# Kernel optimization log

Measured on AMD Instinct MI355X. Metric: run time of the kernel, lower is better.

## Reference

```python
import jax, jax.numpy as jnp
import numpy as np

B, T, N, F, H = 64, 50, 24, 256, 256  # batch, timesteps, graph nodes, input feat, hidden


def setup_inputs() -> dict:
    key = jax.random.key(0)
    ks = jax.random.split(key, 12)
    sF = 1.0 / np.sqrt(F)
    sH = 1.0 / np.sqrt(H)
    u = lambda k, shape, s: jax.random.uniform(k, shape, jnp.float32, -s, s)
    return {
        "x": jax.random.normal(ks[0], (B, T, N, F), jnp.float32),
        "G": jax.random.normal(ks[1], (N, N), jnp.float32) / np.sqrt(N),
        "W_ih": u(ks[2], (4 * H, F), sF),
        "b_ih": u(ks[3], (4 * H,), sF),
        "W_hh": u(ks[4], (4 * H, H), sH),
        "b_hh": u(ks[5], (4 * H,), sH),
        "W_h1": u(ks[6], (H, F), sF),
        "b_h1": u(ks[7], (H,), sF),
        "W_h2": u(ks[8], (H, F), sF),
        "b_h2": u(ks[9], (H,), sF),
        "W_fc": u(ks[10], (H, H), sH),
        "b_fc": u(ks[11], (H,), sH),
    }


def graph_linear(G, x, W, b):
    # GraphLinear: node-mixing G then feature projection W, bias after mixing
    # x: [B, N, f_in] -> [B, N, f_out]
    return jnp.einsum('nm,bmf->bnf', G, x @ W.T) + b


def reference(x, G, W_ih, b_ih, W_hh, b_hh, W_h1, b_h1, W_h2, b_h2, W_fc, b_fc):
    x0 = x[:, 0]                                   # [B, N, F]
    h = graph_linear(G, x0, W_h1, b_h1)            # initial hidden
    c = graph_linear(G, x0, W_h2, b_h2)            # initial cell

    def step(carry, xt):
        h, c = carry
        gates = (graph_linear(G, xt, W_ih, b_ih)
                 + graph_linear(G, h, W_hh, b_hh))  # [B, N, 4H]
        i, f, g, o = jnp.split(gates, 4, axis=-1)
        c = jax.nn.sigmoid(f) * c + jax.nn.sigmoid(i) * jnp.tanh(g)
        h = jax.nn.sigmoid(o) * jnp.tanh(c)
        return (h, c), None

    (h, c), _ = jax.lax.scan(step, (h, c), jnp.swapaxes(x, 0, 1))  # scan over T
    # dropout(p=0.0) is identity; final projection + tanh on last timestep output
    return jnp.tanh(graph_linear(G, h, W_fc, b_fc))
```

## Files before the change

kernel.cpp:

```cpp
#include <hip/hip_runtime.h>
#include <stdint.h>

#define T_ 50

typedef float f32x4 __attribute__((ext_vector_type(4)));
typedef short s16x8 __attribute__((ext_vector_type(8)));
typedef uint64_t u64x2 __attribute__((ext_vector_type(2)));

#define WS_WIH   0u
#define WS_WHH   524288u
#define WS_WINIT 1048576u
#define WS_WFC   1310720u
#define WS_GPAD  1441792u
#define WS_FLG   1443840u
#define WS_NEED  1460224u

#define L_WHH  0
#define L_A2   131072
#define L_XL   143360
#define L_ZR   155840
#define L_HST  156352
#define L_HST2 160448
#define L_TOT  163520

__device__ __forceinline__ f32x4 mfma16(s16x8 a, s16x8 b, f32x4 c){
  return __builtin_amdgcn_mfma_f32_16x16x32_bf16(a, b, c, 0, 0, 0);
}
__device__ __forceinline__ uint32_t bfbits(float f){
  uint32_t u = __builtin_bit_cast(uint32_t, f);
  u += 0x7FFFu + ((u >> 16) & 1u);
  return u >> 16;
}
__device__ __forceinline__ uint32_t pk2bf(float lo, float hi){
  return bfbits(lo) | (bfbits(hi) << 16);
}
#define LOG2E 1.4426950408889634f
__device__ __forceinline__ float fexp2(float x){ return __builtin_amdgcn_exp2f(x); }
__device__ __forceinline__ float frcp_(float x){ return __builtin_amdgcn_rcpf(x); }
__device__ __forceinline__ float fsig(float x){ return frcp_(1.f + fexp2(-LOG2E * x)); }
__device__ __forceinline__ float ftanh_(float x){ return 1.f - 2.f * frcp_(1.f + fexp2(2.f * LOG2E * x)); }

__global__ void prep_kernel(const float* __restrict__ G,
                            const float* __restrict__ Wih, const float* __restrict__ Whh,
                            const float* __restrict__ Wh1, const float* __restrict__ Wh2,
                            const float* __restrict__ Wfc, uint8_t* __restrict__ ws)
{
  const int tid = blockIdx.x * blockDim.x + threadIdx.x;
  const int nth = gridDim.x * blockDim.x;
  uint16_t* wih = (uint16_t*)(ws + WS_WIH);
  uint16_t* whh = (uint16_t*)(ws + WS_WHH);
  uint16_t* wini= (uint16_t*)(ws + WS_WINIT);
  uint16_t* wfc = (uint16_t*)(ws + WS_WFC);
  uint16_t* gp  = (uint16_t*)(ws + WS_GPAD);
  uint32_t* flg = (uint32_t*)(ws + WS_FLG);

  for (int i = tid; i < 262144; i += nth){
    int cg = i >> 16, c = (i >> 8) & 255, k = i & 255;
    int row = (c >> 6)*256 + 64*cg + (c & 63);
    wih[i] = (uint16_t)bfbits(Wih[row*256 + k]);
    whh[i] = (uint16_t)bfbits(Whh[row*256 + k]);
  }
  for (int i = tid; i < 131072; i += nth){
    int cg = i >> 15, c = (i >> 8) & 127, k = i & 255;
    float v = (c < 64) ? Wh1[(64*cg + c)*256 + k] : Wh2[(64*cg + c - 64)*256 + k];
    wini[i] = (uint16_t)bfbits(v);
  }
  for (int i = tid; i < 65536; i += nth){
    int cg = i >> 14, c = (i >> 8) & 63, k = i & 255;
    wfc[i] = (uint16_t)bfbits(Wfc[(64*cg + c)*256 + k]);
  }
  for (int i = tid; i < 1024; i += nth){
    int n = i >> 5, m = i & 31;
    gp[i] = (n < 24 && m < 24) ? (uint16_t)bfbits(G[n*24 + m]) : (uint16_t)0;
  }
  for (int i = tid; i < 4096; i += nth) flg[i] = 0;
}

__global__ void __launch_bounds__(512, 1)
encoder_kernel(const float* __restrict__ x, uint8_t* __restrict__ ws,
               float* __restrict__ out,
               const float* __restrict__ bih, const float* __restrict__ bhh,
               const float* __restrict__ bh1, const float* __restrict__ bh2,
               const float* __restrict__ bfc)
{
  extern __shared__ uint8_t smem[];
  uint16_t* WHHL = (uint16_t*)(smem + L_WHH);
  uint16_t* A2   = (uint16_t*)(smem + L_A2);
  uint16_t* XL   = (uint16_t*)(smem + L_XL);
  uint16_t* ZR   = (uint16_t*)(smem + L_ZR);
  uint16_t* HST  = (uint16_t*)(smem + L_HST);
  uint16_t* HST2 = (uint16_t*)(smem + L_HST2);

  const int tid = threadIdx.x;
  const int b   = blockIdx.x & 63;
  const int cg  = blockIdx.x >> 6;
  const int w   = tid >> 6;
  const int l   = tid & 63;
  const int l15 = l & 15;
  const int g   = l >> 4;
  const int Mt  = w >> 2;
  const int ns  = w & 3;
  const int ul  = ns*16 + l15;
  const int ug  = 64*cg + ul;

  const uint16_t* WIH  = (const uint16_t*)(ws + WS_WIH)   + (size_t)cg*65536;
  const uint16_t* WINI = (const uint16_t*)(ws + WS_WINIT) + (size_t)cg*32768;
  const uint16_t* WFC  = (const uint16_t*)(ws + WS_WFC)   + (size_t)cg*16384;
  const uint16_t* GP   = (const uint16_t*)(ws + WS_GPAD);
  uint32_t* flgB = (uint32_t*)(ws + WS_FLG) + b*64;
  uint32_t* flgW = flgB + cg*16;
  uint16_t* GhB  = (uint16_t*)((uint8_t*)out + (size_t)b*24576);

  {
    const uint8_t* src = ws + WS_WHH + (size_t)cg*131072;
    for (int i = tid*8; i < 65536; i += 4096){
      uint4 v = *(const uint4*)(src + (size_t)i*2);
      int col = i >> 8, k0 = i & 255;
      *(uint4*)&WHHL[col*256 + (k0 ^ ((col&7)<<3))] = v;
    }
  }
  for (int i = tid; i < 256;  i += 512) ZR[i] = 0;
  for (int i = tid; i < 2048; i += 512) HST[i] = 0;

  s16x8 gfragM = *(const s16x8*)&GP[(Mt*16 + l15)*32 + g*8];

  const float bb0 = bih[ug]     + bhh[ug];
  const float bb1 = bih[256+ug] + bhh[256+ug];
  const float bb2 = bih[512+ug] + bhh[512+ug];
  const float bb3 = bih[768+ug] + bhh[768+ug];
  const float bh1l = bh1[ug], bh2l = bh2[ug], bfcl = bfc[ug];

  const int arow = Mt*16 + l15;
  const int crow = (arow < 24) ? arow : 23;
  const uint16_t* a2row = (arow < 24) ? (A2 + arow*256) : ZR;
  const int sw = (arow < 24) ? ((arow & 7) << 3) : 0;

  auto xld_issue = [&](const float* xt, f32x4 xv[3]){
    #pragma unroll
    for (int p = 0; p < 3; p++)
      xv[p] = *(const f32x4*)(xt + tid*4 + p*2048);
  };
  auto xld_write = [&](const f32x4 xv[3]){
    #pragma unroll
    for (int p = 0; p < 3; p++){
      int e = tid*4 + p*2048;
      int m = e >> 8, f = e & 255;
      uint2 pk; pk.x = pk2bf(xv[p][0], xv[p][1]); pk.y = pk2bf(xv[p][2], xv[p][3]);
      *(uint2*)&XL[m*260 + f] = pk;
    }
  };

  auto gx_stage = [&](){
    #pragma unroll
    for (int jt = 0; jt < 4; jt++){
      int f = (jt*4 + ns)*16 + l15;
      s16x8 bfrag = (s16x8){0,0,0,0,0,0,0,0};
      if (g < 3){
        #pragma unroll
        for (int j = 0; j < 8; j++)
          bfrag[j] = (short)XL[(g*8 + j)*260 + f];
      }
      f32x4 zz = {0.f,0.f,0.f,0.f};
      f32x4 gx = mfma16(gfragM, bfrag, zz);
      int n0 = Mt*16 + g*4;
      if (n0 < 24){
        uint32_t a01 = pk2bf(gx[0], gx[1]), a23 = pk2bf(gx[2], gx[3]);
        A2[(n0  )*256 + (f ^ (((n0  )&7)<<3))] = (uint16_t)a01;
        A2[(n0+1)*256 + (f ^ (((n0+1)&7)<<3))] = (uint16_t)(a01>>16);
        A2[(n0+2)*256 + (f ^ (((n0+2)&7)<<3))] = (uint16_t)a23;
        A2[(n0+3)*256 + (f ^ (((n0+3)&7)<<3))] = (uint16_t)(a23>>16);
      }
    }
  };

  auto ghload = [&](int parity, unsigned long long af[8][2]){
    const unsigned long long* gs = (const unsigned long long*)(GhB + parity*6144);
    #pragma unroll
    for (int ks = 0; ks < 8; ks++){
      int e = crow*64 + ks*8 + g*2;
      af[ks][0] = __hip_atomic_load(gs + e,     __ATOMIC_RELAXED, __HIP_MEMORY_SCOPE_AGENT);
      af[ks][1] = __hip_atomic_load(gs + e + 1, __ATOMIC_RELAXED, __HIP_MEMORY_SCOPE_AGENT);
    }
  };

  auto wait_for = [&](uint32_t target){
    if (tid < 4){
      uint32_t* fp = flgB + tid*16;
      int guard = 0;
      while (__hip_atomic_load(fp, __ATOMIC_RELAXED, __HIP_MEMORY_SCOPE_AGENT) < target){
        __builtin_amdgcn_s_sleep(1);
        if (++guard > 20000000) break;
      }
    }
    __syncthreads();
  };

  auto do_publish = [&](const float hv[4], int parity, uint32_t flagval){
    int n0 = Mt*16 + g*4;
    if (n0 < 24){
      uint2 p; p.x = pk2bf(hv[0], hv[1]); p.y = pk2bf(hv[2], hv[3]);
      *(uint2*)&HST[ul*32 + n0] = p;
    }
    __syncthreads();
    s16x8 hb = *(const s16x8*)&HST[ul*32 + g*8];
    f32x4 zz = {0.f,0.f,0.f,0.f};
    f32x4 gh = mfma16(gfragM, hb, zz);
    if (n0 < 24){
      uint32_t q01 = pk2bf(gh[0], gh[1]), q23 = pk2bf(gh[2], gh[3]);
      HST2[(n0  )*64 + ul] = (uint16_t)q01;
      HST2[(n0+1)*64 + ul] = (uint16_t)(q01>>16);
      HST2[(n0+2)*64 + ul] = (uint16_t)q23;
      HST2[(n0+3)*64 + ul] = (uint16_t)(q23>>16);
    }
    __syncthreads();
    if (tid < 384){
      int node = tid >> 4, c4 = tid & 15;
      unsigned long long v = *(const unsigned long long*)&HST2[node*64 + c4*4];
      __hip_atomic_store((unsigned long long*)(GhB + parity*6144) + node*64 + cg*16 + c4,
                         v, __ATOMIC_RELAXED, __HIP_MEMORY_SCOPE_AGENT);
    }
    asm volatile("s_waitcnt vmcnt(0)" ::: "memory");
    __syncthreads();
    if (tid == 0)
      __hip_atomic_store(flgW, flagval, __ATOMIC_RELAXED, __HIP_MEMORY_SCOPE_AGENT);
  };

  float cst[4];
  f32x4 zacc[4];
  const float* xb = x + (size_t)b*T_*6144;

  {
    f32x4 xv[3];
    xld_issue(xb, xv);
    xld_write(xv);
  }
  __syncthreads();
  gx_stage();
  __syncthreads();
  {
    f32x4 h0a = {0.f,0.f,0.f,0.f}, c0a = {0.f,0.f,0.f,0.f};
    #pragma unroll
    for (int j = 0; j < 4; j++) zacc[j] = (f32x4){0.f,0.f,0.f,0.f};
    #pragma unroll
    for (int ks = 0; ks < 8; ks++){
      const int kk = ks*32 + g*8;
      s16x8 a  = *(const s16x8*)&a2row[kk ^ sw];
      s16x8 b1 = *(const s16x8*)&WINI[ul*256 + kk];
      s16x8 b2 = *(const s16x8*)&WINI[(64+ul)*256 + kk];
      h0a = mfma16(a, b1, h0a);
      c0a = mfma16(a, b2, c0a);
      #pragma unroll
      for (int j = 0; j < 4; j++){
        s16x8 bz = *(const s16x8*)&WIH[((j*4+ns)*16 + l15)*256 + kk];
        zacc[j] = mfma16(a, bz, zacc[j]);
      }
    }
    float hv0[4];
    #pragma unroll
    for (int r = 0; r < 4; r++){
      cst[r] = c0a[r] + bh2l;
      hv0[r] = h0a[r] + bh1l;
    }
    do_publish(hv0, 1, 1u);
  }
  {
    f32x4 xv[3];
    xld_issue(xb + 6144, xv);
    xld_write(xv);
    __syncthreads();
    gx_stage();
  }

  for (int t = 0; t < T_; t++){
    wait_for((uint32_t)(t+1));
    unsigned long long af[8][2];
    ghload((t+1)&1, af);

    f32x4 uacc[4];
    #pragma unroll
    for (int j = 0; j < 4; j++) uacc[j] = zacc[j];
    #pragma unroll
    for (int ks = 0; ks < 8; ks++){
      const int kk = ks*32 + g*8;
      u64x2 q; q.x = af[ks][0]; q.y = af[ks][1];
      s16x8 a = __builtin_bit_cast(s16x8, q);
      #pragma unroll
      for (int j = 0; j < 4; j++){
        int col = (j*4+ns)*16 + l15;
        s16x8 bf = *(const s16x8*)&WHHL[col*256 + (kk ^ ((col&7)<<3))];
        uacc[j] = mfma16(a, bf, uacc[j]);
      }
    }
    float hv[4];
    #pragma unroll
    for (int r = 0; r < 4; r++){
      float ig = fsig  (uacc[0][r] + bb0);
      float fg = fsig  (uacc[1][r] + bb1);
      float gg = ftanh_(uacc[2][r] + bb2);
      float og = fsig  (uacc[3][r] + bb3);
      float c  = fg*cst[r] + ig*gg;
      cst[r] = c;
      hv[r] = og*ftanh_(c);
    }
    do_publish(hv, t & 1, (uint32_t)(t+2));

    if (t+1 < T_){
      int tn = (t+2 < T_) ? (t+2) : (T_-1);
      f32x4 xv[3];
      xld_issue(xb + (size_t)tn*6144, xv);
      #pragma unroll
      for (int j = 0; j < 4; j++) zacc[j] = (f32x4){0.f,0.f,0.f,0.f};
      #pragma unroll
      for (int ks = 0; ks < 8; ks++){
        const int kk = ks*32 + g*8;
        s16x8 a = *(const s16x8*)&a2row[kk ^ sw];
        #pragma unroll
        for (int j = 0; j < 4; j++){
          s16x8 bf = *(const s16x8*)&WIH[((j*4+ns)*16 + l15)*256 + kk];
          zacc[j] = mfma16(a, bf, zacc[j]);
        }
      }
      __syncthreads();
      xld_write(xv);
      __syncthreads();
      gx_stage();
    }
  }

  wait_for((uint32_t)(T_+1));
  unsigned long long af[8][2];
  ghload(1, af);
  asm volatile("s_waitcnt vmcnt(0)" ::: "memory");
  __syncthreads();
  if (tid == 0)
    __hip_atomic_store(flgW, (uint32_t)(T_+2), __ATOMIC_RELAXED, __HIP_MEMORY_SCOPE_AGENT);
  wait_for((uint32_t)(T_+2));
  {
    f32x4 oacc = {0.f,0.f,0.f,0.f};
    #pragma unroll
    for (int ks = 0; ks < 8; ks++){
      const int kk = ks*32 + g*8;
      u64x2 q; q.x = af[ks][0]; q.y = af[ks][1];
      s16x8 a  = __builtin_bit_cast(s16x8, q);
      s16x8 bf = *(const s16x8*)&WFC[ul*256 + kk];
      oacc = mfma16(a, bf, oacc);
    }
    int n0 = Mt*16 + g*4;
    if (n0 < 24){
      #pragma unroll
      for (int r = 0; r < 4; r++)
        out[(size_t)b*6144 + (n0+r)*256 + ug] = ftanh_(oacc[r] + bfcl);
    }
  }
}

extern "C" void kernel_launch(void* const* d_in, const int* in_sizes, int n_in,
                              void* d_out, int out_size, void* d_ws, size_t ws_size,
                              hipStream_t stream)
{
  (void)in_sizes; (void)n_in; (void)out_size;
  if (ws_size < WS_NEED) return;

  const float* x   = (const float*)d_in[0];
  const float* G   = (const float*)d_in[1];
  const float* Wih = (const float*)d_in[2];
  const float* bih = (const float*)d_in[3];
  const float* Whh = (const float*)d_in[4];
  const float* bhh = (const float*)d_in[5];
  const float* Wh1 = (const float*)d_in[6];
  const float* bh1 = (const float*)d_in[7];
  const float* Wh2 = (const float*)d_in[8];
  const float* bh2 = (const float*)d_in[9];
  const float* Wfc = (const float*)d_in[10];
  const float* bfc = (const float*)d_in[11];
  uint8_t* ws = (uint8_t*)d_ws;
  float* outp = (float*)d_out;

  hipLaunchKernelGGL(prep_kernel, dim3(256), dim3(256), 0, stream,
                     G, Wih, Whh, Wh1, Wh2, Wfc, ws);

  hipFuncSetAttribute((const void*)encoder_kernel,
                      hipFuncAttributeMaxDynamicSharedMemorySize, L_TOT);
  void* args[] = {(void*)&x, (void*)&ws, (void*)&outp,
                  (void*)&bih, (void*)&bhh, (void*)&bh1, (void*)&bh2, (void*)&bfc};
  hipLaunchCooperativeKernel((const void*)encoder_kernel, dim3(256), dim3(512),
                             args, L_TOT, stream);
}
```

Measured before the change: 677.8 us.

## Replace flag-based inter-block sync with tagged per-element hidden-state exchange

Drops the separate flag array and the wait/publish barriers. Each published G·h value is now stored as a 32-bit word holding the bf16 value plus a step tag, so consumers poll the data itself until every tag matches. This removes the two __syncthreads, the vmcnt wait and the flag round-trip from each recurrent step, and it speculatively issues the next loads early. In exchange it doubles the exchange traffic, uses a larger workspace buffer zeroed in prep, and adds wave-wide tag checks and 32 loads per lane on every poll.

```diff
diff --git a/kernel.cpp b/kernel.cpp
--- a/kernel.cpp
+++ b/kernel.cpp
@@ -5,23 +5,21 @@
 
 typedef float f32x4 __attribute__((ext_vector_type(4)));
 typedef short s16x8 __attribute__((ext_vector_type(8)));
-typedef uint64_t u64x2 __attribute__((ext_vector_type(2)));
 
 #define WS_WIH   0u
 #define WS_WHH   524288u
 #define WS_WINIT 1048576u
 #define WS_WFC   1310720u
 #define WS_GPAD  1441792u
-#define WS_FLG   1443840u
-#define WS_NEED  1460224u
+#define WS_GHT   1443840u
+#define WS_NEED  4589568u
 
 #define L_WHH  0
 #define L_A2   131072
 #define L_XL   143360
 #define L_ZR   155840
 #define L_HST  156352
-#define L_HST2 160448
-#define L_TOT  163520
+#define L_TOT  160448
 
 __device__ __forceinline__ f32x4 mfma16(s16x8 a, s16x8 b, f32x4 c){
   return __builtin_amdgcn_mfma_f32_16x16x32_bf16(a, b, c, 0, 0, 0);
@@ -52,7 +50,7 @@
   uint16_t* wini= (uint16_t*)(ws + WS_WINIT);
   uint16_t* wfc = (uint16_t*)(ws + WS_WFC);
   uint16_t* gp  = (uint16_t*)(ws + WS_GPAD);
-  uint32_t* flg = (uint32_t*)(ws + WS_FLG);
+  uint32_t* ght = (uint32_t*)(ws + WS_GHT);
 
   for (int i = tid; i < 262144; i += nth){
     int cg = i >> 16, c = (i >> 8) & 255, k = i & 255;
@@ -73,7 +71,7 @@
     int n = i >> 5, m = i & 31;
     gp[i] = (n < 24 && m < 24) ? (uint16_t)bfbits(G[n*24 + m]) : (uint16_t)0;
   }
-  for (int i = tid; i < 4096; i += nth) flg[i] = 0;
+  for (int i = tid; i < 786432; i += nth) ght[i] = 0;
 }
 
 __global__ void __launch_bounds__(512, 1)
@@ -89,7 +87,6 @@
   uint16_t* XL   = (uint16_t*)(smem + L_XL);
   uint16_t* ZR   = (uint16_t*)(smem + L_ZR);
   uint16_t* HST  = (uint16_t*)(smem + L_HST);
-  uint16_t* HST2 = (uint16_t*)(smem + L_HST2);
 
   const int tid = threadIdx.x;
   const int b   = blockIdx.x & 63;
@@ -107,9 +104,7 @@
   const uint16_t* WINI = (const uint16_t*)(ws + WS_WINIT) + (size_t)cg*32768;
   const uint16_t* WFC  = (const uint16_t*)(ws + WS_WFC)   + (size_t)cg*16384;
   const uint16_t* GP   = (const uint16_t*)(ws + WS_GPAD);
-  uint32_t* flgB = (uint32_t*)(ws + WS_FLG) + b*64;
-  uint32_t* flgW = flgB + cg*16;
-  uint16_t* GhB  = (uint16_t*)((uint8_t*)out + (size_t)b*24576);
+  uint32_t* GhT = (uint32_t*)(ws + WS_GHT) + (size_t)b*12288;
 
   {
     const uint8_t* src = ws + WS_WHH + (size_t)cg*131072;
@@ -173,29 +168,38 @@
     }
   };
 
-  auto ghload = [&](int parity, unsigned long long af[8][2]){
-    const unsigned long long* gs = (const unsigned long long*)(GhB + parity*6144);
+  auto issueGh = [&](unsigned long long wv[32], int parity){
+    const unsigned long long* gs = (const unsigned long long*)(GhT + parity*6144);
     #pragma unroll
     for (int ks = 0; ks < 8; ks++){
-      int e = crow*64 + ks*8 + g*2;
-      af[ks][0] = __hip_atomic_load(gs + e,     __ATOMIC_RELAXED, __HIP_MEMORY_SCOPE_AGENT);
-      af[ks][1] = __hip_atomic_load(gs + e + 1, __ATOMIC_RELAXED, __HIP_MEMORY_SCOPE_AGENT);
-    }
-  };
-
-  auto wait_for = [&](uint32_t target){
-    if (tid < 4){
-      uint32_t* fp = flgB + tid*16;
-      int guard = 0;
-      while (__hip_atomic_load(fp, __ATOMIC_RELAXED, __HIP_MEMORY_SCOPE_AGENT) < target){
-        __builtin_amdgcn_s_sleep(1);
-        if (++guard > 20000000) break;
-      }
-    }
-    __syncthreads();
-  };
-
-  auto do_publish = [&](const float hv[4], int parity, uint32_t flagval){
+      int e = (crow*256 + ks*32 + g*8) >> 1;
+      #pragma unroll
+      for (int q = 0; q < 4; q++)
+        wv[ks*4+q] = __hip_atomic_load(gs + e + q, __ATOMIC_RELAXED, __HIP_MEMORY_SCOPE_AGENT);
+    }
+  };
+  auto checkGh = [&](const unsigned long long wv[32], uint32_t ktag)->bool{
+    uint32_t bad = 0;
+    #pragma unroll
+    for (int i = 0; i < 32; i++){
+      bad |= (((uint32_t)wv[i]) ^ ktag) & 0xFFFFu;
+      bad |= (((uint32_t)(wv[i] >> 32)) ^ ktag) & 0xFFFFu;
+    }
+    return !__any((int)(bad != 0));
+  };
+  auto pollGh = [&](unsigned long long wv[32], int parity, uint32_t ktag){
+    int guard = 0;
+    while (!checkGh(wv, ktag)){
+      __builtin_amdgcn_s_sleep(1);
+      issueGh(wv, parity);
+      if (++guard > 1000000) break;
+    }
+  };
+  auto mkpair = [](unsigned long long wv_)->uint32_t{
+    return (uint32_t)((wv_ >> 16) & 0xFFFFull) | (uint32_t)((wv_ >> 32) & 0xFFFF0000ull);
+  };
+
+  auto do_publish = [&](const float hv[4], int parity, uint32_t ktag){
     int n0 = Mt*16 + g*4;
     if (n0 < 24){
       uint2 p; p.x = pk2bf(hv[0], hv[1]); p.y = pk2bf(hv[2], hv[3]);
@@ -205,28 +209,20 @@
     s16x8 hb = *(const s16x8*)&HST[ul*32 + g*8];
     f32x4 zz = {0.f,0.f,0.f,0.f};
     f32x4 gh = mfma16(gfragM, hb, zz);
+    uint32_t* gd = GhT + parity*6144;
     if (n0 < 24){
-      uint32_t q01 = pk2bf(gh[0], gh[1]), q23 = pk2bf(gh[2], gh[3]);
-      HST2[(n0  )*64 + ul] = (uint16_t)q01;
-      HST2[(n0+1)*64 + ul] = (uint16_t)(q01>>16);
-      HST2[(n0+2)*64 + ul] = (uint16_t)q23;
-      HST2[(n0+3)*64 + ul] = (uint16_t)(q23>>16);
-    }
-    __syncthreads();
-    if (tid < 384){
-      int node = tid >> 4, c4 = tid & 15;
-      unsigned long long v = *(const unsigned long long*)&HST2[node*64 + c4*4];
-      __hip_atomic_store((unsigned long long*)(GhB + parity*6144) + node*64 + cg*16 + c4,
-                         v, __ATOMIC_RELAXED, __HIP_MEMORY_SCOPE_AGENT);
-    }
-    asm volatile("s_waitcnt vmcnt(0)" ::: "memory");
-    __syncthreads();
-    if (tid == 0)
-      __hip_atomic_store(flgW, flagval, __ATOMIC_RELAXED, __HIP_MEMORY_SCOPE_AGENT);
+      #pragma unroll
+      for (int r = 0; r < 4; r++){
+        uint32_t wv_ = (bfbits(gh[r]) << 16) | ktag;
+        __hip_atomic_store(gd + (n0+r)*256 + ug, wv_,
+                           __ATOMIC_RELAXED, __HIP_MEMORY_SCOPE_AGENT);
+      }
+    }
   };
 
   float cst[4];
   f32x4 zacc[4];
+  unsigned long long wv[32];
   const float* xb = x + (size_t)b*T_*6144;
 
   {
@@ -261,7 +257,7 @@
       cst[r] = c0a[r] + bh2l;
       hv0[r] = h0a[r] + bh1l;
     }
-    do_publish(hv0, 1, 1u);
+    do_publish(hv0, 1, 2u);
   }
   {
     f32x4 xv[3];
@@ -270,11 +266,10 @@
     __syncthreads();
     gx_stage();
   }
+  issueGh(wv, 1);
 
   for (int t = 0; t < T_; t++){
-    wait_for((uint32_t)(t+1));
-    unsigned long long af[8][2];
-    ghload((t+1)&1, af);
+    pollGh(wv, (t+1)&1, (uint32_t)(t+2));
 
     f32x4 uacc[4];
     #pragma unroll
@@ -282,7 +277,9 @@
     #pragma unroll
     for (int ks = 0; ks < 8; ks++){
       const int kk = ks*32 + g*8;
-      u64x2 q; q.x = af[ks][0]; q.y = af[ks][1];
+      uint4 q;
+      q.x = mkpair(wv[ks*4+0]); q.y = mkpair(wv[ks*4+1]);
+      q.z = mkpair(wv[ks*4+2]); q.w = mkpair(wv[ks*4+3]);
       s16x8 a = __builtin_bit_cast(s16x8, q);
       #pragma unroll
       for (int j = 0; j < 4; j++){
@@ -302,7 +299,7 @@
       cst[r] = c;
       hv[r] = og*ftanh_(c);
     }
-    do_publish(hv, t & 1, (uint32_t)(t+2));
+    do_publish(hv, t & 1, (uint32_t)(t+3));
 
     if (t+1 < T_){
       int tn = (t+2 < T_) ? (t+2) : (T_-1);
@@ -325,22 +322,18 @@
       __syncthreads();
       gx_stage();
     }
-  }
-
-  wait_for((uint32_t)(T_+1));
-  unsigned long long af[8][2];
-  ghload(1, af);
-  asm volatile("s_waitcnt vmcnt(0)" ::: "memory");
-  __syncthreads();
-  if (tid == 0)
-    __hip_atomic_store(flgW, (uint32_t)(T_+2), __ATOMIC_RELAXED, __HIP_MEMORY_SCOPE_AGENT);
-  wait_for((uint32_t)(T_+2));
+    issueGh(wv, t & 1);
+  }
+
+  pollGh(wv, 1, (uint32_t)(T_+2));
   {
     f32x4 oacc = {0.f,0.f,0.f,0.f};
     #pragma unroll
     for (int ks = 0; ks < 8; ks++){
       const int kk = ks*32 + g*8;
-      u64x2 q; q.x = af[ks][0]; q.y = af[ks][1];
+      uint4 q;
+      q.x = mkpair(wv[ks*4+0]); q.y = mkpair(wv[ks*4+1]);
+      q.z = mkpair(wv[ks*4+2]); q.w = mkpair(wv[ks*4+3]);
       s16x8 a  = __builtin_bit_cast(s16x8, q);
       s16x8 bf = *(const s16x8*)&WFC[ul*256 + kk];
       oacc = mfma16(a, bf, oacc);
```

New measurement: 814.2 us. +20.1%, slower.

## Run one workgroup per batch element, removing cross-block flag synchronisation

Applied to the files above, without the earlier changes.

The hidden dimension was split across four cooperating workgroups per batch element, which exchanged the mixed hidden state through global memory with atomic flags each timestep. Now each batch element is handled by a single 1024-thread workgroup covering all 256 hidden units, so the exchange happens in LDS with __syncthreads. W_hh is no longer cached in LDS and is read from global memory (through L2) every step, and the launch becomes a normal 64-block grid instead of a cooperative launch. This removes inter-block polling latency but uses only 64 CUs and adds per-step global weight traffic.

```diff
diff --git a/kernel.cpp b/kernel.cpp
--- a/kernel.cpp
+++ b/kernel.cpp
@@ -3,25 +3,23 @@
 
 #define T_ 50
 
+typedef float f32x2 __attribute__((ext_vector_type(2)));
 typedef float f32x4 __attribute__((ext_vector_type(4)));
 typedef short s16x8 __attribute__((ext_vector_type(8)));
-typedef uint64_t u64x2 __attribute__((ext_vector_type(2)));
 
 #define WS_WIH   0u
 #define WS_WHH   524288u
 #define WS_WINIT 1048576u
 #define WS_WFC   1310720u
 #define WS_GPAD  1441792u
-#define WS_FLG   1443840u
-#define WS_NEED  1460224u
-
-#define L_WHH  0
-#define L_A2   131072
-#define L_XL   143360
-#define L_ZR   155840
-#define L_HST  156352
-#define L_HST2 160448
-#define L_TOT  163520
+#define WS_NEED  1443840u
+
+#define L_A1   0
+#define L_A2   24576
+#define L_XL   49152
+#define L_ZR   61696
+#define L_HST  62208
+#define L_TOT  78592
 
 __device__ __forceinline__ f32x4 mfma16(s16x8 a, s16x8 b, f32x4 c){
   return __builtin_amdgcn_mfma_f32_16x16x32_bf16(a, b, c, 0, 0, 0);
@@ -52,185 +50,129 @@
   uint16_t* wini= (uint16_t*)(ws + WS_WINIT);
   uint16_t* wfc = (uint16_t*)(ws + WS_WFC);
   uint16_t* gp  = (uint16_t*)(ws + WS_GPAD);
-  uint32_t* flg = (uint32_t*)(ws + WS_FLG);
 
   for (int i = tid; i < 262144; i += nth){
-    int cg = i >> 16, c = (i >> 8) & 255, k = i & 255;
-    int row = (c >> 6)*256 + 64*cg + (c & 63);
-    wih[i] = (uint16_t)bfbits(Wih[row*256 + k]);
-    whh[i] = (uint16_t)bfbits(Whh[row*256 + k]);
+    wih[i] = (uint16_t)bfbits(Wih[i]);
+    whh[i] = (uint16_t)bfbits(Whh[i]);
   }
   for (int i = tid; i < 131072; i += nth){
-    int cg = i >> 15, c = (i >> 8) & 127, k = i & 255;
-    float v = (c < 64) ? Wh1[(64*cg + c)*256 + k] : Wh2[(64*cg + c - 64)*256 + k];
+    int n = i >> 8, k = i & 255;
+    float v = (n < 256) ? Wh1[n*256 + k] : Wh2[(n-256)*256 + k];
     wini[i] = (uint16_t)bfbits(v);
   }
-  for (int i = tid; i < 65536; i += nth){
-    int cg = i >> 14, c = (i >> 8) & 63, k = i & 255;
-    wfc[i] = (uint16_t)bfbits(Wfc[(64*cg + c)*256 + k]);
-  }
+  for (int i = tid; i < 65536; i += nth)
+    wfc[i] = (uint16_t)bfbits(Wfc[i]);
   for (int i = tid; i < 1024; i += nth){
     int n = i >> 5, m = i & 31;
     gp[i] = (n < 24 && m < 24) ? (uint16_t)bfbits(G[n*24 + m]) : (uint16_t)0;
   }
-  for (int i = tid; i < 4096; i += nth) flg[i] = 0;
-}
-
-__global__ void __launch_bounds__(512, 1)
-encoder_kernel(const float* __restrict__ x, uint8_t* __restrict__ ws,
+}
+
+__global__ void __launch_bounds__(1024, 4)
+encoder_kernel(const float* __restrict__ x, const uint8_t* __restrict__ ws,
                float* __restrict__ out,
                const float* __restrict__ bih, const float* __restrict__ bhh,
                const float* __restrict__ bh1, const float* __restrict__ bh2,
                const float* __restrict__ bfc)
 {
   extern __shared__ uint8_t smem[];
-  uint16_t* WHHL = (uint16_t*)(smem + L_WHH);
-  uint16_t* A2   = (uint16_t*)(smem + L_A2);
-  uint16_t* XL   = (uint16_t*)(smem + L_XL);
-  uint16_t* ZR   = (uint16_t*)(smem + L_ZR);
-  uint16_t* HST  = (uint16_t*)(smem + L_HST);
-  uint16_t* HST2 = (uint16_t*)(smem + L_HST2);
+  uint16_t* A1  = (uint16_t*)(smem + L_A1);
+  uint16_t* A2  = (uint16_t*)(smem + L_A2);
+  uint16_t* XL  = (uint16_t*)(smem + L_XL);
+  uint16_t* ZR  = (uint16_t*)(smem + L_ZR);
+  uint16_t* HST = (uint16_t*)(smem + L_HST);
 
   const int tid = threadIdx.x;
-  const int b   = blockIdx.x & 63;
-  const int cg  = blockIdx.x >> 6;
+  const int b   = blockIdx.x;
   const int w   = tid >> 6;
   const int l   = tid & 63;
   const int l15 = l & 15;
   const int g   = l >> 4;
-  const int Mt  = w >> 2;
-  const int ns  = w & 3;
-  const int ul  = ns*16 + l15;
-  const int ug  = 64*cg + ul;
-
-  const uint16_t* WIH  = (const uint16_t*)(ws + WS_WIH)   + (size_t)cg*65536;
-  const uint16_t* WINI = (const uint16_t*)(ws + WS_WINIT) + (size_t)cg*32768;
-  const uint16_t* WFC  = (const uint16_t*)(ws + WS_WFC)   + (size_t)cg*16384;
+  const int u   = w*16 + l15;
+
+  const uint16_t* WIH  = (const uint16_t*)(ws + WS_WIH);
+  const uint16_t* WHH  = (const uint16_t*)(ws + WS_WHH);
+  const uint16_t* WINI = (const uint16_t*)(ws + WS_WINIT);
+  const uint16_t* WFC  = (const uint16_t*)(ws + WS_WFC);
   const uint16_t* GP   = (const uint16_t*)(ws + WS_GPAD);
-  uint32_t* flgB = (uint32_t*)(ws + WS_FLG) + b*64;
-  uint32_t* flgW = flgB + cg*16;
-  uint16_t* GhB  = (uint16_t*)((uint8_t*)out + (size_t)b*24576);
+
+  for (int i = tid; i < 256;  i += 1024) ZR[i] = 0;
+  for (int i = tid; i < 8192; i += 1024) HST[i] = 0;
+
+  s16x8 gfragM[2];
+  gfragM[0] = *(const s16x8*)&GP[(l15     )*32 + g*8];
+  gfragM[1] = *(const s16x8*)&GP[(l15 + 16)*32 + g*8];
+
+  const float bb0 = bih[u]     + bhh[u];
+  const float bb1 = bih[256+u] + bhh[256+u];
+  const float bb2 = bih[512+u] + bhh[512+u];
+  const float bb3 = bih[768+u] + bhh[768+u];
+  const float bh1l = bh1[u], bh2l = bh2[u], bfcl = bfc[u];
+
+  const int r1v = (16 + l15) < 24;
+  const uint16_t* a1r[2] = { A1 + l15*256, r1v ? (A1 + (16+l15)*256) : ZR };
+  const uint16_t* a2r[2] = { A2 + l15*256, r1v ? (A2 + (16+l15)*256) : ZR };
+  const int swz[2] = { (l15 & 7) << 3, r1v ? (((16+l15) & 7) << 3) : 0 };
+
+  auto xld_issue = [&](const float* xt, f32x2 xv[3]){
+    #pragma unroll
+    for (int p = 0; p < 3; p++)
+      xv[p] = *(const f32x2*)(xt + tid*2 + p*2048);
+  };
+  auto xld_write = [&](const f32x2 xv[3]){
+    #pragma unroll
+    for (int p = 0; p < 3; p++){
+      int e = tid*2 + p*2048;
+      int m = e >> 8, f = e & 255;
+      *(uint32_t*)&XL[m*260 + f] = pk2bf(xv[p][0], xv[p][1]);
+    }
+  };
+
+  auto gx_stage = [&](){
+    s16x8 bfrag = (s16x8){0,0,0,0,0,0,0,0};
+    if (g < 3){
+      #pragma unroll
+      for (int j = 0; j < 8; j++)
+        bfrag[j] = (short)XL[(g*8 + j)*260 + u];
+    }
+    #pragma unroll
+    for (int Mt = 0; Mt < 2; Mt++){
+      f32x4 zz = {0.f,0.f,0.f,0.f};
+      f32x4 gx = mfma16(gfragM[Mt], bfrag, zz);
+      int n0 = Mt*16 + g*4;
+      if (n0 < 24){
+        uint32_t a01 = pk2bf(gx[0], gx[1]), a23 = pk2bf(gx[2], gx[3]);
+        A2[(n0  )*256 + (u ^ (((n0  )&7)<<3))] = (uint16_t)a01;
+        A2[(n0+1)*256 + (u ^ (((n0+1)&7)<<3))] = (uint16_t)(a01>>16);
+        A2[(n0+2)*256 + (u ^ (((n0+2)&7)<<3))] = (uint16_t)a23;
+        A2[(n0+3)*256 + (u ^ (((n0+3)&7)<<3))] = (uint16_t)(a23>>16);
+      }
+    }
+  };
+
+  auto gh_stage = [&](){
+    s16x8 hb = *(const s16x8*)&HST[u*32 + g*8];
+    #pragma unroll
+    for (int Mt = 0; Mt < 2; Mt++){
+      f32x4 zz = {0.f,0.f,0.f,0.f};
+      f32x4 gh = mfma16(gfragM[Mt], hb, zz);
+      int n0 = Mt*16 + g*4;
+      if (n0 < 24){
+        uint32_t a01 = pk2bf(gh[0], gh[1]), a23 = pk2bf(gh[2], gh[3]);
+        A1[(n0  )*256 + (u ^ (((n0  )&7)<<3))] = (uint16_t)a01;
+        A1[(n0+1)*256 + (u ^ (((n0+1)&7)<<3))] = (uint16_t)(a01>>16);
+        A1[(n0+2)*256 + (u ^ (((n0+2)&7)<<3))] = (uint16_t)a23;
+        A1[(n0+3)*256 + (u ^ (((n0+3)&7)<<3))] = (uint16_t)(a23>>16);
+      }
+    }
+  };
+
+  float cst[2][4];
+  f32x4 acc[4][2];
+  const float* xb = x + (size_t)b * T_ * 6144;
 
   {
-    const uint8_t* src = ws + WS_WHH + (size_t)cg*131072;
-    for (int i = tid*8; i < 65536; i += 4096){
-      uint4 v = *(const uint4*)(src + (size_t)i*2);
-      int col = i >> 8, k0 = i & 255;
-      *(uint4*)&WHHL[col*256 + (k0 ^ ((col&7)<<3))] = v;
-    }
-  }
-  for (int i = tid; i < 256;  i += 512) ZR[i] = 0;
-  for (int i = tid; i < 2048; i += 512) HST[i] = 0;
-
-  s16x8 gfragM = *(const s16x8*)&GP[(Mt*16 + l15)*32 + g*8];
-
-  const float bb0 = bih[ug]     + bhh[ug];
-  const float bb1 = bih[256+ug] + bhh[256+ug];
-  const float bb2 = bih[512+ug] + bhh[512+ug];
-  const float bb3 = bih[768+ug] + bhh[768+ug];
-  const float bh1l = bh1[ug], bh2l = bh2[ug], bfcl = bfc[ug];
-
-  const int arow = Mt*16 + l15;
-  const int crow = (arow < 24) ? arow : 23;
-  const uint16_t* a2row = (arow < 24) ? (A2 + arow*256) : ZR;
-  const int sw = (arow < 24) ? ((arow & 7) << 3) : 0;
-
-  auto xld_issue = [&](const float* xt, f32x4 xv[3]){
-    #pragma unroll
-    for (int p = 0; p < 3; p++)
-      xv[p] = *(const f32x4*)(xt + tid*4 + p*2048);
-  };
-  auto xld_write = [&](const f32x4 xv[3]){
-    #pragma unroll
-    for (int p = 0; p < 3; p++){
-      int e = tid*4 + p*2048;
-      int m = e >> 8, f = e & 255;
-      uint2 pk; pk.x = pk2bf(xv[p][0], xv[p][1]); pk.y = pk2bf(xv[p][2], xv[p][3]);
-      *(uint2*)&XL[m*260 + f] = pk;
-    }
-  };
-
-  auto gx_stage = [&](){
-    #pragma unroll
-    for (int jt = 0; jt < 4; jt++){
-      int f = (jt*4 + ns)*16 + l15;
-      s16x8 bfrag = (s16x8){0,0,0,0,0,0,0,0};
-      if (g < 3){
-        #pragma unroll
-        for (int j = 0; j < 8; j++)
-          bfrag[j] = (short)XL[(g*8 + j)*260 + f];
-      }
-      f32x4 zz = {0.f,0.f,0.f,0.f};
-      f32x4 gx = mfma16(gfragM, bfrag, zz);
-      int n0 = Mt*16 + g*4;
-      if (n0 < 24){
-        uint32_t a01 = pk2bf(gx[0], gx[1]), a23 = pk2bf(gx[2], gx[3]);
-        A2[(n0  )*256 + (f ^ (((n0  )&7)<<3))] = (uint16_t)a01;
-        A2[(n0+1)*256 + (f ^ (((n0+1)&7)<<3))] = (uint16_t)(a01>>16);
-        A2[(n0+2)*256 + (f ^ (((n0+2)&7)<<3))] = (uint16_t)a23;
-        A2[(n0+3)*256 + (f ^ (((n0+3)&7)<<3))] = (uint16_t)(a23>>16);
-      }
-    }
-  };
-
-  auto ghload = [&](int parity, unsigned long long af[8][2]){
-    const unsigned long long* gs = (const unsigned long long*)(GhB + parity*6144);
-    #pragma unroll
-    for (int ks = 0; ks < 8; ks++){
-      int e = crow*64 + ks*8 + g*2;
-      af[ks][0] = __hip_atomic_load(gs + e,     __ATOMIC_RELAXED, __HIP_MEMORY_SCOPE_AGENT);
-      af[ks][1] = __hip_atomic_load(gs + e + 1, __ATOMIC_RELAXED, __HIP_MEMORY_SCOPE_AGENT);
-    }
-  };
-
-  auto wait_for = [&](uint32_t target){
-    if (tid < 4){
-      uint32_t* fp = flgB + tid*16;
-      int guard = 0;
-      while (__hip_atomic_load(fp, __ATOMIC_RELAXED, __HIP_MEMORY_SCOPE_AGENT) < target){
-        __builtin_amdgcn_s_sleep(1);
-        if (++guard > 20000000) break;
-      }
-    }
-    __syncthreads();
-  };
-
-  auto do_publish = [&](const float hv[4], int parity, uint32_t flagval){
-    int n0 = Mt*16 + g*4;
-    if (n0 < 24){
-      uint2 p; p.x = pk2bf(hv[0], hv[1]); p.y = pk2bf(hv[2], hv[3]);
-      *(uint2*)&HST[ul*32 + n0] = p;
-    }
-    __syncthreads();
-    s16x8 hb = *(const s16x8*)&HST[ul*32 + g*8];
-    f32x4 zz = {0.f,0.f,0.f,0.f};
-    f32x4 gh = mfma16(gfragM, hb, zz);
-    if (n0 < 24){
-      uint32_t q01 = pk2bf(gh[0], gh[1]), q23 = pk2bf(gh[2], gh[3]);
-      HST2[(n0  )*64 + ul] = (uint16_t)q01;
-      HST2[(n0+1)*64 + ul] = (uint16_t)(q01>>16);
-      HST2[(n0+2)*64 + ul] = (uint16_t)q23;
-      HST2[(n0+3)*64 + ul] = (uint16_t)(q23>>16);
-    }
-    __syncthreads();
-    if (tid < 384){
-      int node = tid >> 4, c4 = tid & 15;
-      unsigned long long v = *(const unsigned long long*)&HST2[node*64 + c4*4];
-      __hip_atomic_store((unsigned long long*)(GhB + parity*6144) + node*64 + cg*16 + c4,
-                         v, __ATOMIC_RELAXED, __HIP_MEMORY_SCOPE_AGENT);
-    }
-    asm volatile("s_waitcnt vmcnt(0)" ::: "memory");
-    __syncthreads();
-    if (tid == 0)
-      __hip_atomic_store(flgW, flagval, __ATOMIC_RELAXED, __HIP_MEMORY_SCOPE_AGENT);
-  };
-
-  float cst[4];
-  f32x4 zacc[4];
-  const float* xb = x + (size_t)b*T_*6144;
-
-  {
-    f32x4 xv[3];
+    f32x2 xv[3];
     xld_issue(xb, xv);
     xld_write(xv);
   }
@@ -238,118 +180,137 @@
   gx_stage();
   __syncthreads();
   {
-    f32x4 h0a = {0.f,0.f,0.f,0.f}, c0a = {0.f,0.f,0.f,0.f};
-    #pragma unroll
-    for (int j = 0; j < 4; j++) zacc[j] = (f32x4){0.f,0.f,0.f,0.f};
-    #pragma unroll
+    f32x4 h0a[2] = {{0,0,0,0},{0,0,0,0}}, c0a[2] = {{0,0,0,0},{0,0,0,0}};
+    #pragma unroll
+    for (int gt = 0; gt < 4; gt++)
+      #pragma unroll
+      for (int Mt = 0; Mt < 2; Mt++) acc[gt][Mt] = (f32x4){0,0,0,0};
+    #pragma unroll 2
     for (int ks = 0; ks < 8; ks++){
       const int kk = ks*32 + g*8;
-      s16x8 a  = *(const s16x8*)&a2row[kk ^ sw];
-      s16x8 b1 = *(const s16x8*)&WINI[ul*256 + kk];
-      s16x8 b2 = *(const s16x8*)&WINI[(64+ul)*256 + kk];
-      h0a = mfma16(a, b1, h0a);
-      c0a = mfma16(a, b2, c0a);
-      #pragma unroll
-      for (int j = 0; j < 4; j++){
-        s16x8 bz = *(const s16x8*)&WIH[((j*4+ns)*16 + l15)*256 + kk];
-        zacc[j] = mfma16(a, bz, zacc[j]);
-      }
-    }
-    float hv0[4];
-    #pragma unroll
-    for (int r = 0; r < 4; r++){
-      cst[r] = c0a[r] + bh2l;
-      hv0[r] = h0a[r] + bh1l;
-    }
-    do_publish(hv0, 1, 1u);
-  }
+      s16x8 a0 = *(const s16x8*)&a2r[0][kk ^ swz[0]];
+      s16x8 a1 = *(const s16x8*)&a2r[1][kk ^ swz[1]];
+      s16x8 b1 = *(const s16x8*)&WINI[u*256 + kk];
+      s16x8 b2 = *(const s16x8*)&WINI[(256+u)*256 + kk];
+      h0a[0] = mfma16(a0, b1, h0a[0]);  h0a[1] = mfma16(a1, b1, h0a[1]);
+      c0a[0] = mfma16(a0, b2, c0a[0]);  c0a[1] = mfma16(a1, b2, c0a[1]);
+      #pragma unroll
+      for (int gt = 0; gt < 4; gt++){
+        s16x8 bz = *(const s16x8*)&WIH[(gt*256 + u)*256 + kk];
+        acc[gt][0] = mfma16(a0, bz, acc[gt][0]);
+        acc[gt][1] = mfma16(a1, bz, acc[gt][1]);
+      }
+    }
+    #pragma unroll
+    for (int Mt = 0; Mt < 2; Mt++){
+      int n0 = Mt*16 + g*4;
+      float hv[4];
+      #pragma unroll
+      for (int r = 0; r < 4; r++){
+        cst[Mt][r] = c0a[Mt][r] + bh2l;
+        hv[r]      = h0a[Mt][r] + bh1l;
+      }
+      if (n0 < 24){
+        uint2 p; p.x = pk2bf(hv[0], hv[1]); p.y = pk2bf(hv[2], hv[3]);
+        *(uint2*)&HST[u*32 + n0] = p;
+      }
+    }
+  }
+  __syncthreads();
+  gh_stage();
   {
-    f32x4 xv[3];
+    f32x2 xv[3];
     xld_issue(xb + 6144, xv);
+    __syncthreads();
     xld_write(xv);
-    __syncthreads();
-    gx_stage();
-  }
+  }
+  __syncthreads();
+  gx_stage();
+  __syncthreads();
 
   for (int t = 0; t < T_; t++){
-    wait_for((uint32_t)(t+1));
-    unsigned long long af[8][2];
-    ghload((t+1)&1, af);
-
-    f32x4 uacc[4];
-    #pragma unroll
-    for (int j = 0; j < 4; j++) uacc[j] = zacc[j];
-    #pragma unroll
+    #pragma unroll 2
     for (int ks = 0; ks < 8; ks++){
       const int kk = ks*32 + g*8;
-      u64x2 q; q.x = af[ks][0]; q.y = af[ks][1];
-      s16x8 a = __builtin_bit_cast(s16x8, q);
-      #pragma unroll
-      for (int j = 0; j < 4; j++){
-        int col = (j*4+ns)*16 + l15;
-        s16x8 bf = *(const s16x8*)&WHHL[col*256 + (kk ^ ((col&7)<<3))];
-        uacc[j] = mfma16(a, bf, uacc[j]);
-      }
-    }
-    float hv[4];
-    #pragma unroll
-    for (int r = 0; r < 4; r++){
-      float ig = fsig  (uacc[0][r] + bb0);
-      float fg = fsig  (uacc[1][r] + bb1);
-      float gg = ftanh_(uacc[2][r] + bb2);
-      float og = fsig  (uacc[3][r] + bb3);
-      float c  = fg*cst[r] + ig*gg;
-      cst[r] = c;
-      hv[r] = og*ftanh_(c);
-    }
-    do_publish(hv, t & 1, (uint32_t)(t+2));
+      s16x8 a0 = *(const s16x8*)&a1r[0][kk ^ swz[0]];
+      s16x8 a1 = *(const s16x8*)&a1r[1][kk ^ swz[1]];
+      #pragma unroll
+      for (int gt = 0; gt < 4; gt++){
+        s16x8 bf = *(const s16x8*)&WHH[(gt*256 + u)*256 + kk];
+        acc[gt][0] = mfma16(a0, bf, acc[gt][0]);
+        acc[gt][1] = mfma16(a1, bf, acc[gt][1]);
+      }
+    }
+    #pragma unroll
+    for (int Mt = 0; Mt < 2; Mt++){
+      int n0 = Mt*16 + g*4;
+      float hv[4];
+      #pragma unroll
+      for (int r = 0; r < 4; r++){
+        float ig = fsig  (acc[0][Mt][r] + bb0);
+        float fg = fsig  (acc[1][Mt][r] + bb1);
+        float gg = ftanh_(acc[2][Mt][r] + bb2);
+        float og = fsig  (acc[3][Mt][r] + bb3);
+        float c  = fg*cst[Mt][r] + ig*gg;
+        cst[Mt][r] = c;
+        hv[r] = og*ftanh_(c);
+      }
+      if (n0 < 24){
+        uint2 p; p.x = pk2bf(hv[0], hv[1]); p.y = pk2bf(hv[2], hv[3]);
+        *(uint2*)&HST[u*32 + n0] = p;
+      }
+    }
+    __syncthreads();
+    gh_stage();
 
     if (t+1 < T_){
       int tn = (t+2 < T_) ? (t+2) : (T_-1);
-      f32x4 xv[3];
+      f32x2 xv[3];
       xld_issue(xb + (size_t)tn*6144, xv);
       #pragma unroll
-      for (int j = 0; j < 4; j++) zacc[j] = (f32x4){0.f,0.f,0.f,0.f};
-      #pragma unroll
+      for (int gt = 0; gt < 4; gt++)
+        #pragma unroll
+        for (int Mt = 0; Mt < 2; Mt++) acc[gt][Mt] = (f32x4){0,0,0,0};
+      #pragma unroll 2
       for (int ks = 0; ks < 8; ks++){
         const int kk = ks*32 + g*8;
-        s16x8 a = *(const s16x8*)&a2row[kk ^ sw];
+        s16x8 a0 = *(const s16x8*)&a2r[0][kk ^ swz[0]];
+        s16x8 a1 = *(const s16x8*)&a2r[1][kk ^ swz[1]];
         #pragma unroll
-        for (int j = 0; j < 4; j++){
-          s16x8 bf = *(const s16x8*)&WIH[((j*4+ns)*16 + l15)*256 + kk];
-          zacc[j] = mfma16(a, bf, zacc[j]);
+        for (int gt = 0; gt < 4; gt++){
+          s16x8 bf = *(const s16x8*)&WIH[(gt*256 + u)*256 + kk];
+          acc[gt][0] = mfma16(a0, bf, acc[gt][0]);
+          acc[gt][1] = mfma16(a1, bf, acc[gt][1]);
         }
       }
       __syncthreads();
       xld_write(xv);
       __syncthreads();
       gx_stage();
-    }
-  }
-
-  wait_for((uint32_t)(T_+1));
-  unsigned long long af[8][2];
-  ghload(1, af);
-  asm volatile("s_waitcnt vmcnt(0)" ::: "memory");
-  __syncthreads();
-  if (tid == 0)
-    __hip_atomic_store(flgW, (uint32_t)(T_+2), __ATOMIC_RELAXED, __HIP_MEMORY_SCOPE_AGENT);
-  wait_for((uint32_t)(T_+2));
+    } else {
+      __syncthreads();
+    }
+  }
+
   {
-    f32x4 oacc = {0.f,0.f,0.f,0.f};
-    #pragma unroll
+    f32x4 oacc[2] = {{0,0,0,0},{0,0,0,0}};
+    #pragma unroll 2
     for (int ks = 0; ks < 8; ks++){
       const int kk = ks*32 + g*8;
-      u64x2 q; q.x = af[ks][0]; q.y = af[ks][1];
-      s16x8 a  = __builtin_bit_cast(s16x8, q);
-      s16x8 bf = *(const s16x8*)&WFC[ul*256 + kk];
-      oacc = mfma16(a, bf, oacc);
-    }
-    int n0 = Mt*16 + g*4;
-    if (n0 < 24){
-      #pragma unroll
-      for (int r = 0; r < 4; r++)
-        out[(size_t)b*6144 + (n0+r)*256 + ug] = ftanh_(oacc[r] + bfcl);
+      s16x8 a0 = *(const s16x8*)&a1r[0][kk ^ swz[0]];
+      s16x8 a1 = *(const s16x8*)&a1r[1][kk ^ swz[1]];
+      s16x8 bf = *(const s16x8*)&WFC[u*256 + kk];
+      oacc[0] = mfma16(a0, bf, oacc[0]);
+      oacc[1] = mfma16(a1, bf, oacc[1]);
+    }
+    #pragma unroll
+    for (int Mt = 0; Mt < 2; Mt++){
+      int n0 = Mt*16 + g*4;
+      if (n0 < 24){
+        #pragma unroll
+        for (int r = 0; r < 4; r++)
+          out[(size_t)b*6144 + (n0+r)*256 + u] = ftanh_(oacc[Mt][r] + bfcl);
+      }
     }
   }
 }
@@ -374,15 +335,13 @@
   const float* Wfc = (const float*)d_in[10];
   const float* bfc = (const float*)d_in[11];
   uint8_t* ws = (uint8_t*)d_ws;
-  float* outp = (float*)d_out;
 
   hipLaunchKernelGGL(prep_kernel, dim3(256), dim3(256), 0, stream,
                      G, Wih, Whh, Wh1, Wh2, Wfc, ws);
 
   hipFuncSetAttribute((const void*)encoder_kernel,
                       hipFuncAttributeMaxDynamicSharedMemorySize, L_TOT);
-  void* args[] = {(void*)&x, (void*)&ws, (void*)&outp,
-                  (void*)&bih, (void*)&bhh, (void*)&bh1, (void*)&bh2, (void*)&bfc};
-  hipLaunchCooperativeKernel((const void*)encoder_kernel, dim3(256), dim3(512),
-                             args, L_TOT, stream);
-}
+  hipLaunchKernelGGL(encoder_kernel, dim3(64), dim3(1024), L_TOT, stream,
+                     x, (const uint8_t*)ws, (float*)d_out,
+                     bih, bhh, bh1, bh2, bfc);
+}
```

After: 1.579 ms. +132.9%, slower.
